# Kernel tuning notes

Hardware: AMD Instinct MI355X
Metric: run time of the kernel (lower is better)

Reference implementation:

```python
import jax, jax.numpy as jnp
import numpy as np

E, V, F, D = 500000, 50000, 100000, 128

def setup_inputs() -> dict:
    key = jax.random.key(0)
    ks = jax.random.split(key, 8)
    return {
        "prev_m_f_to_v": jax.random.normal(ks[0], (E, D), jnp.float32),
        "variable": jax.random.normal(ks[1], (V, D), jnp.float32),
        "factor": jax.random.normal(ks[2], (F, D), jnp.float32),
        "edge_attr": jax.random.normal(ks[3], (E, D), jnp.float32),
        "v_to_f": jax.random.randint(ks[4], (E,), 0, V, jnp.int32),
        "f_to_v": jax.random.randint(ks[5], (E,), 0, F, jnp.int32),
        "Wv": jax.random.normal(ks[6], (3 * D, D), jnp.float32) * (1.0 / np.sqrt(3 * D)),
        "bv": jnp.zeros((D,), jnp.float32),
        "Wf": jax.random.normal(ks[7], (3 * D, D), jnp.float32) * (1.0 / np.sqrt(3 * D)),
        "bf": jnp.zeros((D,), jnp.float32),
    }

def _mlp(x, y, edge_attr, W, b):
    # update(): concat along features then Linear(3d->d) + relu
    h = jnp.concatenate((x, y, edge_attr), axis=-1)  # [E, 3D]
    return jax.nn.relu(h @ W + b)                    # [E, D]

def reference(prev_m_f_to_v, variable, factor, edge_attr, v_to_f, f_to_v, Wv, bv, Wf, bf):
    nV = variable.shape[0]
    nF = factor.shape[0]
    # scatter-sum of factor->variable messages onto variables
    sum_f_to_v = jax.ops.segment_sum(prev_m_f_to_v, v_to_f, num_segments=nV)  # [V, D]
    # BP exclusion: gather back and subtract own message
    m_v_to_f = sum_f_to_v[v_to_f] - prev_m_f_to_v                             # [E, D]
    m_v_to_f = _mlp(variable[v_to_f], m_v_to_f, edge_attr, Wv, bv)            # [E, D]
    # scatter-sum of variable->factor messages onto factors
    sum_v_to_f = jax.ops.segment_sum(m_v_to_f, f_to_v, num_segments=nF)       # [F, D]
    m_f_to_v = sum_v_to_f[f_to_v] - m_v_to_f                                  # [E, D]
    m_f_to_v = _mlp(factor[f_to_v], m_f_to_v, edge_attr, Wf, bf)              # [E, D]
    new_factor = sum_v_to_f + factor
    new_variable = sum_f_to_v + variable
    return (m_f_to_v, new_factor, new_variable)
```

## Files before the change

### kernel.cpp

```cpp
#include <hip/hip_runtime.h>

typedef __attribute__((ext_vector_type(8))) __bf16 bf16x8;
typedef __attribute__((ext_vector_type(4))) __bf16 bf16x4;
typedef __attribute__((ext_vector_type(2))) __bf16 bf16x2;
typedef __attribute__((ext_vector_type(4))) float f32x4;

template <int N> struct ic { static constexpr int value = N; };

__device__ __forceinline__ void gload_lds16(const void* g, void* l) {
    __builtin_amdgcn_global_load_lds(
        (const __attribute__((address_space(1))) void*)g,
        (__attribute__((address_space(3))) void*)l, 16, 0, 0);
}

__device__ inline bf16x8 pack8(f32x4 u0, f32x4 u1) {
    bf16x8 r;
    r[0] = (__bf16)u0[0]; r[1] = (__bf16)u0[1]; r[2] = (__bf16)u0[2]; r[3] = (__bf16)u0[3];
    r[4] = (__bf16)u1[0]; r[5] = (__bf16)u1[1]; r[6] = (__bf16)u1[2]; r[7] = (__bf16)u1[3];
    return r;
}

__global__ void pack_all(const float* __restrict__ Wv, const float* __restrict__ Wf,
                         __bf16* __restrict__ Wtab_v, __bf16* __restrict__ Wedge_v,
                         __bf16* __restrict__ Wtab_f, __bf16* __restrict__ Wedge_f) {
    int which = blockIdx.x >> 7;
    int i = ((blockIdx.x & 127) << 8) + threadIdx.x;
    const float* W = (which < 2) ? Wv : Wf;
    __bf16* out = (which == 0) ? Wtab_v : (which == 1) ? Wedge_v
                 : (which == 2) ? Wtab_f : Wedge_f;
    int baseA = (which & 1) ? 128 : 0;
    float sA  = (which & 1) ? -1.f : 1.f;
    int baseB = (which & 1) ? 256 : 128;
    int k = i >> 7, d = i & 127;
    float v = (k < 128) ? sA * W[(long)(baseA + k) * 128 + d]
                        : W[(long)(baseB + (k - 128)) * 128 + d];
    int t = k >> 5, n = d >> 4;
    int lane = (d & 15) | (((k >> 3) & 3) << 4);
    int j = k & 7;
    out[((long)(t * 8 + n) * 64 + lane) * 8 + j] = (__bf16)v;
}


__global__ void hist_kernel(const int* __restrict__ v_to_f, const int* __restrict__ f_to_v,
                            int* __restrict__ counts, int V, int E) {
    int stride = gridDim.x * blockDim.x;
    for (int e = blockIdx.x * blockDim.x + threadIdx.x; e < E; e += stride) {
        atomicAdd(&counts[v_to_f[e]], 1);
        atomicAdd(&counts[V + f_to_v[e]], 1);
    }
}

#define SCAN_BLOCK 256
#define SCAN_ELEMS 4

__global__ void scan_pass1(const int* __restrict__ counts, int* __restrict__ partials, int N) {
    int t = threadIdx.x;
    int base = blockIdx.x * (SCAN_BLOCK * SCAN_ELEMS) + t * SCAN_ELEMS;
    int s = 0;
#pragma unroll
    for (int j = 0; j < SCAN_ELEMS; ++j) {
        int i = base + j;
        if (i < N) s += counts[i];
    }
#pragma unroll
    for (int off = 1; off < 64; off <<= 1) s += __shfl_xor(s, off);
    __shared__ int lds[4];
    if ((t & 63) == 0) lds[t >> 6] = s;
    __syncthreads();
    if (t == 0) partials[blockIdx.x] = lds[0] + lds[1] + lds[2] + lds[3];
}

__global__ void scan_pass3(const int* __restrict__ counts, const int* __restrict__ partials,
                           int* __restrict__ offsets, int* __restrict__ cursors,
                           int N, int total) {
    int t = threadIdx.x;
    int pre = 0;
    for (int i = 0; i < (int)blockIdx.x; ++i) pre += partials[i];
    int base = blockIdx.x * (SCAN_BLOCK * SCAN_ELEMS) + t * SCAN_ELEMS;
    int c[SCAN_ELEMS];
    int s = 0;
#pragma unroll
    for (int j = 0; j < SCAN_ELEMS; ++j) {
        int i = base + j;
        c[j] = (i < N) ? counts[i] : 0;
        s += c[j];
    }
    int lane = t & 63, w = t >> 6;
    int x = s;
#pragma unroll
    for (int off = 1; off < 64; off <<= 1) { int y = __shfl_up(x, off); if (lane >= off) x += y; }
    __shared__ int lds[4];
    if (lane == 63) lds[w] = x;
    __syncthreads();
    int add = 0;
    for (int i = 0; i < w; ++i) add += lds[i];
    int run = x + add - s + pre;
#pragma unroll
    for (int j = 0; j < SCAN_ELEMS; ++j) {
        int i = base + j;
        if (i < N) { offsets[i] = run; cursors[i] = run; }
        run += c[j];
    }
    if (blockIdx.x == 0 && t == 0) offsets[N] = total;
}

__global__ void fill_kernel(const int* __restrict__ v_to_f, const int* __restrict__ f_to_v,
                            int* __restrict__ cursors, int* __restrict__ bucket, int V, int E) {
    int stride = gridDim.x * blockDim.x;
    for (int e = blockIdx.x * blockDim.x + threadIdx.x; e < E; e += stride) {
        int p = atomicAdd(&cursors[v_to_f[e]], 1);
        bucket[p] = e;
        int q = atomicAdd(&cursors[V + f_to_v[e]], 1);
        bucket[q] = e;
    }
}


__global__ __launch_bounds__(256) void gsum_f32(
    const float* __restrict__ src, const int* __restrict__ bucket,
    const int* __restrict__ offsets, int toff,
    const float* __restrict__ addtab, float* __restrict__ sumout,
    float* __restrict__ addout, int T) {
    int gw = (int)((blockIdx.x * (long)blockDim.x + threadIdx.x) >> 6);
    if (gw >= T) return;
    int lane = threadIdx.x & 63;
    int start = offsets[toff + gw], end = offsets[toff + gw + 1];
    float ax = 0.f, ay = 0.f, bx = 0.f, by = 0.f;
    float cx = 0.f, cy = 0.f, dx = 0.f, dy = 0.f;
    int i = start;
    for (; i + 3 < end; i += 4) {
        int e0 = bucket[i], e1 = bucket[i + 1], e2 = bucket[i + 2], e3 = bucket[i + 3];
        float2 v0 = *(const float2*)(src + (long)e0 * 128 + lane * 2);
        float2 v1 = *(const float2*)(src + (long)e1 * 128 + lane * 2);
        float2 v2 = *(const float2*)(src + (long)e2 * 128 + lane * 2);
        float2 v3 = *(const float2*)(src + (long)e3 * 128 + lane * 2);
        ax += v0.x; ay += v0.y; bx += v1.x; by += v1.y;
        cx += v2.x; cy += v2.y; dx += v3.x; dy += v3.y;
    }
    for (; i < end; ++i) {
        int e0 = bucket[i];
        float2 v0 = *(const float2*)(src + (long)e0 * 128 + lane * 2);
        ax += v0.x; ay += v0.y;
    }
    ax += bx + cx + dx; ay += by + cy + dy;
    long o = (long)gw * 128 + lane * 2;
    *(float2*)(sumout + o) = make_float2(ax, ay);
    float2 a = *(const float2*)(addtab + o);
    *(float2*)(addout + o) = make_float2(ax + a.x, ay + a.y);
}

__global__ __launch_bounds__(256) void gsum_bf16(
    const __bf16* __restrict__ src, const int* __restrict__ bucket,
    const int* __restrict__ offsets, int toff,
    const float* __restrict__ addtab, float* __restrict__ sumout,
    float* __restrict__ addout, int T) {
    int gw = (int)((blockIdx.x * (long)blockDim.x + threadIdx.x) >> 6);
    if (gw >= T) return;
    int lane = threadIdx.x & 63;
    int start = offsets[toff + gw], end = offsets[toff + gw + 1];
    float ax = 0.f, ay = 0.f, bx = 0.f, by = 0.f;
    float cx = 0.f, cy = 0.f, dx = 0.f, dy = 0.f;
    int i = start;
    for (; i + 3 < end; i += 4) {
        int e0 = bucket[i], e1 = bucket[i + 1], e2 = bucket[i + 2], e3 = bucket[i + 3];
        bf16x2 v0 = *(const bf16x2*)(src + (long)e0 * 128 + lane * 2);
        bf16x2 v1 = *(const bf16x2*)(src + (long)e1 * 128 + lane * 2);
        bf16x2 v2 = *(const bf16x2*)(src + (long)e2 * 128 + lane * 2);
        bf16x2 v3 = *(const bf16x2*)(src + (long)e3 * 128 + lane * 2);
        ax += (float)v0[0]; ay += (float)v0[1]; bx += (float)v1[0]; by += (float)v1[1];
        cx += (float)v2[0]; cy += (float)v2[1]; dx += (float)v3[0]; dy += (float)v3[1];
    }
    for (; i < end; ++i) {
        int e0 = bucket[i];
        bf16x2 v0 = *(const bf16x2*)(src + (long)e0 * 128 + lane * 2);
        ax += (float)v0[0]; ay += (float)v0[1];
    }
    ax += bx + cx + dx; ay += by + cy + dy;
    long o = (long)gw * 128 + lane * 2;
    *(float2*)(sumout + o) = make_float2(ax, ay);
    float2 a = *(const float2*)(addtab + o);
    *(float2*)(addout + o) = make_float2(ax + a.x, ay + a.y);
}

__global__ __launch_bounds__(256, 4) void table_gemm(
    const float* __restrict__ src0, const float* __restrict__ src1,
    const __bf16* __restrict__ WT, const float* __restrict__ bias,
    __bf16* __restrict__ out, int T) {
    const int wave = threadIdx.x >> 6;
    const int lane = threadIdx.x & 63;
    const int row = lane & 15;
    const int kch = lane >> 4;
    const long wbase = ((long)blockIdx.x * 4 + wave) * 32;

    const float* p0[2]; const float* p1[2];
#pragma unroll
    for (int rb = 0; rb < 2; ++rb) {
        long r = wbase + rb * 16 + row;
        long rl = (r < T) ? r : (T - 1);
        p0[rb] = src0 + rl * 128 + kch * 8;
        p1[rb] = src1 + rl * 128 + kch * 8;
    }

    f32x4 acc[8][2];
#pragma unroll
    for (int n = 0; n < 8; ++n) {
        acc[n][0] = (f32x4){0.f, 0.f, 0.f, 0.f};
        acc[n][1] = (f32x4){0.f, 0.f, 0.f, 0.f};
    }

#pragma unroll
    for (int t = 0; t < 8; ++t) {
        bf16x8 a[2];
#pragma unroll
        for (int rb = 0; rb < 2; ++rb) {
            const float* p = (t < 4) ? (p0[rb] + t * 32) : (p1[rb] + (t - 4) * 32);
            f32x4 u0 = *(const f32x4*)p;
            f32x4 u1 = *(const f32x4*)(p + 4);
            a[rb] = pack8(u0, u1);
        }
        const __bf16* bbase = WT + (long)t * 8 * 512 + lane * 8;
#pragma unroll
        for (int n = 0; n < 8; ++n) {
            bf16x8 b = *(const bf16x8*)(bbase + n * 512);
            acc[n][0] = __builtin_amdgcn_mfma_f32_16x16x32_bf16(a[0], b, acc[n][0], 0, 0, 0);
            acc[n][1] = __builtin_amdgcn_mfma_f32_16x16x32_bf16(a[1], b, acc[n][1], 0, 0, 0);
        }
    }

    const int colbase = lane & 15;
    const int orow = (lane >> 4) * 4;
#pragma unroll
    for (int n = 0; n < 8; ++n) {
        int col = n * 16 + colbase;
        float bz = bias[col];
#pragma unroll
        for (int rb = 0; rb < 2; ++rb)
#pragma unroll
            for (int rr = 0; rr < 4; ++rr) {
                long r = wbase + rb * 16 + orow + rr;
                if (r < T) out[r * 128 + col] = (__bf16)(acc[n][rb][rr] + bz);
            }
    }
}

template <int PHASE>
__global__ __launch_bounds__(256, 3) void edge_gemm(
    const float* __restrict__ prevf, const __bf16* __restrict__ prevb,
    const float* __restrict__ eattr, const __bf16* __restrict__ WT,
    const __bf16* __restrict__ G, const int* __restrict__ idx,
    __bf16* __restrict__ outb, float* __restrict__ outf, int E) {
    __shared__ char lds[4][12288];
    const int wave = threadIdx.x >> 6;
    const int lane = threadIdx.x & 63;
    const int l16 = lane & 15;
    const int kch = lane >> 4;
    const long brow = (long)blockIdx.x * 128;
    const long wrow = brow + wave * 32;
    char* wls = &lds[wave][0];

    bf16x8 bufA[8], bufB[8];
    f32x4 acc[8][2];
#pragma unroll
    for (int n = 0; n < 8; ++n) {
        acc[n][0] = (f32x4){0.f, 0.f, 0.f, 0.f};
        acc[n][1] = (f32x4){0.f, 0.f, 0.f, 0.f};
    }

    auto stage = [&](auto tcS) {
        constexpr int S = decltype(tcS)::value;
        char* dst = wls + (S % 3) * 4096;
        if constexpr (PHASE == 2 && S < 4) {
#pragma unroll
            for (int q = 0; q < 2; ++q) {
                int row = q * 16 + (lane >> 2);
                int c2 = (lane & 3) ^ ((row >> 1) & 3);
                long rg = wrow + row; if (rg >= E) rg = E - 1;
                gload_lds16(prevb + rg * 128 + S * 32 + c2 * 8, dst + q * 1024);
            }
        } else {
            const float* srcb = (PHASE == 1 && S < 4) ? (prevf + S * 32)
                                                      : (eattr + (S - 4) * 32);
#pragma unroll
            for (int q = 0; q < 4; ++q) {
                int row = q * 8 + (lane >> 3);
                int c2 = (lane & 7) ^ (row & 7);
                long rg = wrow + row; if (rg >= E) rg = E - 1;
                gload_lds16(srcb + rg * 128 + c2 * 4, dst + q * 1024);
            }
        }
    };

    auto loadB = [&](auto tcT, bf16x8* bn) {
        constexpr int T = decltype(tcT)::value;
        const __bf16* bb = WT + (long)T * 4096 + lane * 8;
#pragma unroll
        for (int n = 0; n < 8; ++n) bn[n] = *(const bf16x8*)(bb + n * 512);
    };

    stage(ic<0>{});
    __builtin_amdgcn_sched_barrier(0);
    loadB(ic<0>{}, bufA);
    __builtin_amdgcn_sched_barrier(0);
    stage(ic<1>{});
    __builtin_amdgcn_sched_barrier(0);

    auto iter = [&](auto tcT) {
        constexpr int T = decltype(tcT)::value;
        constexpr int NS = (T < 7) ? (8 + ((PHASE == 2 && (T + 1) < 4) ? 2 : 4)) : 8;
        asm volatile("s_waitcnt vmcnt(%0)" :: "n"(NS) : "memory");
        __builtin_amdgcn_sched_barrier(0);
        if constexpr (T < 7) loadB(ic<T + 1>{}, (T & 1) ? bufA : bufB);
        __builtin_amdgcn_sched_barrier(0);
        if constexpr (T < 6) stage(ic<T + 2>{});
        __builtin_amdgcn_sched_barrier(0);
        const char* cur = wls + (T % 3) * 4096;
        bf16x8 a[2];
#pragma unroll
        for (int rb = 0; rb < 2; ++rb) {
            int row = rb * 16 + l16;
            if constexpr (PHASE == 2 && T < 4) {
                a[rb] = *(const bf16x8*)(cur + row * 64 + ((kch ^ ((row >> 1) & 3)) * 16));
            } else {
                f32x4 u0 = *(const f32x4*)(cur + row * 128 + (((kch * 2) ^ (row & 7)) * 16));
                f32x4 u1 = *(const f32x4*)(cur + row * 128 + (((kch * 2 + 1) ^ (row & 7)) * 16));
                a[rb] = pack8(u0, u1);
            }
        }
        bf16x8* bc = (T & 1) ? bufB : bufA;
#pragma unroll
        for (int n = 0; n < 8; ++n) {
            acc[n][0] = __builtin_amdgcn_mfma_f32_16x16x32_bf16(a[0], bc[n], acc[n][0], 0, 0, 0);
            acc[n][1] = __builtin_amdgcn_mfma_f32_16x16x32_bf16(a[1], bc[n], acc[n][1], 0, 0, 0);
        }
    };
    iter(ic<0>{}); iter(ic<1>{}); iter(ic<2>{}); iter(ic<3>{});
    iter(ic<4>{}); iter(ic<5>{}); iter(ic<6>{}); iter(ic<7>{});

    float* lbuf = (float*)wls;
    const int slotcol = lane & 31;
    const int rhalf = lane >> 5;
#pragma unroll
    for (int rb = 0; rb < 2; ++rb) {
#pragma unroll
        for (int n = 0; n < 8; ++n)
#pragma unroll
            for (int rr = 0; rr < 4; ++rr) {
                int row = kch * 4 + rr;
                int col = n * 16 + l16;
                int slot = col >> 2;
                lbuf[row * 128 + (((slot ^ (row & 7)) << 2) | (col & 3))] = acc[n][rb][rr];
            }
#pragma unroll
        for (int j = 0; j < 8; ++j) {
            int row = 2 * j + rhalf;
            long eo = wrow + rb * 16 + row;
            f32x4 v = *(const f32x4*)&lbuf[row * 128 + ((slotcol ^ (row & 7)) << 2)];
            if (eo < E) {
                int g = idx[eo];
                bf16x4 gb = *(const bf16x4*)(G + (long)g * 128 + slotcol * 4);
                f32x4 o;
#pragma unroll
                for (int i = 0; i < 4; ++i) {
                    float x = v[i] + (float)gb[i];
                    o[i] = x > 0.f ? x : 0.f;
                }
                if (PHASE == 1) {
                    bf16x4 ob;
#pragma unroll
                    for (int i = 0; i < 4; ++i) ob[i] = (__bf16)o[i];
                    *(bf16x4*)(outb + eo * 128 + slotcol * 4) = ob;
                } else {
                    *(f32x4*)(outf + eo * 128 + slotcol * 4) = o;
                }
            }
        }
    }
}

extern "C" void kernel_launch(void* const* d_in, const int* in_sizes, int n_in,
                              void* d_out, int out_size, void* d_ws, size_t ws_size,
                              hipStream_t stream) {
    const float* prev_m   = (const float*)d_in[0];
    const float* variable = (const float*)d_in[1];
    const float* factor   = (const float*)d_in[2];
    const float* eattr    = (const float*)d_in[3];
    const int*   v_to_f   = (const int*)d_in[4];
    const int*   f_to_v   = (const int*)d_in[5];
    const float* Wv       = (const float*)d_in[6];
    const float* bv       = (const float*)d_in[7];
    const float* Wf       = (const float*)d_in[8];
    const float* bf       = (const float*)d_in[9];

    const int E = in_sizes[0] / 128;
    const int V = in_sizes[1] / 128;
    const int F = in_sizes[2] / 128;
    const int NT = V + F;

    float* out_m        = (float*)d_out;
    float* out_factor   = out_m + (long)E * 128;
    float* out_variable = out_factor + (long)F * 128;

    char* ws = (char*)d_ws;
    float* sum_f_to_v = (float*)ws;  ws += (long)V * 128 * 4;
    float* sum_v_to_f = (float*)ws;  ws += (long)F * 128 * 4;
    __bf16* m1        = (__bf16*)ws; ws += (long)E * 128 * 2;
    __bf16* G1        = (__bf16*)ws; ws += (long)V * 128 * 2;
    __bf16* G2        = (__bf16*)ws; ws += (long)F * 128 * 2;
    __bf16* Wtab_v    = (__bf16*)ws; ws += 256 * 128 * 2;
    __bf16* Wedge_v   = (__bf16*)ws; ws += 256 * 128 * 2;
    __bf16* Wtab_f    = (__bf16*)ws; ws += 256 * 128 * 2;
    __bf16* Wedge_f   = (__bf16*)ws; ws += 256 * 128 * 2;
    int* counts       = (int*)ws;    ws += (long)NT * 4;
    int* offsets      = (int*)ws;    ws += (long)(NT + 1) * 4;
    int* cursors      = (int*)ws;    ws += (long)NT * 4;
    int* bucket       = (int*)ws;    ws += (long)2 * E * 4;
    int* partials     = (int*)ws;    ws += 256 * 4;

    hipMemsetAsync(counts, 0, (size_t)NT * 4, stream);

    pack_all<<<dim3(512), dim3(256), 0, stream>>>(Wv, Wf, Wtab_v, Wedge_v, Wtab_f, Wedge_f);

    hist_kernel<<<dim3(2048), dim3(256), 0, stream>>>(v_to_f, f_to_v, counts, V, E);
    int nb = (NT + SCAN_BLOCK * SCAN_ELEMS - 1) / (SCAN_BLOCK * SCAN_ELEMS);
    scan_pass1<<<dim3(nb), dim3(SCAN_BLOCK), 0, stream>>>(counts, partials, NT);
    scan_pass3<<<dim3(nb), dim3(SCAN_BLOCK), 0, stream>>>(counts, partials, offsets, cursors,
                                                          NT, 2 * E);
    fill_kernel<<<dim3(2048), dim3(256), 0, stream>>>(v_to_f, f_to_v, cursors, bucket, V, E);

    gsum_f32<<<dim3((V + 3) / 4), dim3(256), 0, stream>>>(
        prev_m, bucket, offsets, 0, variable, sum_f_to_v, out_variable, V);

    table_gemm<<<dim3((V + 127) / 128), dim3(256), 0, stream>>>(
        variable, sum_f_to_v, Wtab_v, bv, G1, V);

    int eblocks = (E + 127) / 128;
    edge_gemm<1><<<dim3(eblocks), dim3(256), 0, stream>>>(
        prev_m, nullptr, eattr, Wedge_v, G1, v_to_f, m1, nullptr, E);

    gsum_bf16<<<dim3((F + 3) / 4), dim3(256), 0, stream>>>(
        m1, bucket, offsets, V, factor, sum_v_to_f, out_factor, F);

    table_gemm<<<dim3((F + 127) / 128), dim3(256), 0, stream>>>(
        factor, sum_v_to_f, Wtab_f, bf, G2, F);

    edge_gemm<2><<<dim3(eblocks), dim3(256), 0, stream>>>(
        nullptr, m1, eattr, Wedge_f, G2, f_to_v, nullptr, out_m, E);
}
```

Measured before the change: 713.4 us.

## Restructure edge GEMM pipeline with inline-asm LDS reads and move table adds

Inside edge_gemm, the A-tile LDS reads are now issued as explicit ds_read_b128 instructions with a single lgkmcnt wait. The B-fragment register loads are moved to after the MFMAs and prefetch two iterations ahead instead of one. Separately, the residual adds (sum + variable/factor) move out of the gather-sum kernels and into the tail of table_gemm, which already reads both sources. The intent is better overlap of global loads with MFMA work and lighter gather kernels. The risks are extra register pressure and a reordered waitcnt schedule in the hot kernel.

```diff
diff --git a/kernel.cpp b/kernel.cpp
--- a/kernel.cpp
+++ b/kernel.cpp
@@ -11,6 +11,22 @@
     __builtin_amdgcn_global_load_lds(
         (const __attribute__((address_space(1))) void*)g,
         (__attribute__((address_space(3))) void*)l, 16, 0, 0);
+}
+
+__device__ __forceinline__ unsigned lds_addr(const void* p) {
+    return (unsigned)(unsigned long long)(__attribute__((address_space(3))) const char*)p;
+}
+
+__device__ __forceinline__ f32x4 ds_read_b128_f(unsigned a) {
+    f32x4 r;
+    asm volatile("ds_read_b128 %0, %1" : "=v"(r) : "v"(a));
+    return r;
+}
+
+__device__ __forceinline__ bf16x8 ds_read_b128_h(unsigned a) {
+    bf16x8 r;
+    asm volatile("ds_read_b128 %0, %1" : "=v"(r) : "v"(a));
+    return r;
 }
 
 __device__ inline bf16x8 pack8(f32x4 u0, f32x4 u1) {
@@ -119,8 +135,7 @@
 __global__ __launch_bounds__(256) void gsum_f32(
     const float* __restrict__ src, const int* __restrict__ bucket,
     const int* __restrict__ offsets, int toff,
-    const float* __restrict__ addtab, float* __restrict__ sumout,
-    float* __restrict__ addout, int T) {
+    float* __restrict__ sumout, int T) {
     int gw = (int)((blockIdx.x * (long)blockDim.x + threadIdx.x) >> 6);
     if (gw >= T) return;
     int lane = threadIdx.x & 63;
@@ -145,15 +160,12 @@
     ax += bx + cx + dx; ay += by + cy + dy;
     long o = (long)gw * 128 + lane * 2;
     *(float2*)(sumout + o) = make_float2(ax, ay);
-    float2 a = *(const float2*)(addtab + o);
-    *(float2*)(addout + o) = make_float2(ax + a.x, ay + a.y);
 }
 
 __global__ __launch_bounds__(256) void gsum_bf16(
     const __bf16* __restrict__ src, const int* __restrict__ bucket,
     const int* __restrict__ offsets, int toff,
-    const float* __restrict__ addtab, float* __restrict__ sumout,
-    float* __restrict__ addout, int T) {
+    float* __restrict__ sumout, int T) {
     int gw = (int)((blockIdx.x * (long)blockDim.x + threadIdx.x) >> 6);
     if (gw >= T) return;
     int lane = threadIdx.x & 63;
@@ -178,14 +190,12 @@
     ax += bx + cx + dx; ay += by + cy + dy;
     long o = (long)gw * 128 + lane * 2;
     *(float2*)(sumout + o) = make_float2(ax, ay);
-    float2 a = *(const float2*)(addtab + o);
-    *(float2*)(addout + o) = make_float2(ax + a.x, ay + a.y);
 }
 
 __global__ __launch_bounds__(256, 4) void table_gemm(
     const float* __restrict__ src0, const float* __restrict__ src1,
     const __bf16* __restrict__ WT, const float* __restrict__ bias,
-    __bf16* __restrict__ out, int T) {
+    __bf16* __restrict__ out, float* __restrict__ addout, int T) {
     const int wave = threadIdx.x >> 6;
     const int lane = threadIdx.x & 63;
     const int row = lane & 15;
@@ -240,6 +250,22 @@
                 long r = wbase + rb * 16 + orow + rr;
                 if (r < T) out[r * 128 + col] = (__bf16)(acc[n][rb][rr] + bz);
             }
+    }
+
+    const long eb = (long)blockIdx.x * 128 * 128;
+#pragma unroll
+    for (int j = 0; j < 16; ++j) {
+        int vec = j * 256 + threadIdx.x;
+        long r = (long)blockIdx.x * 128 + (vec >> 5);
+        if (r < T) {
+            long off = eb + (long)vec * 4;
+            f32x4 x = *(const f32x4*)(src0 + off);
+            f32x4 y = *(const f32x4*)(src1 + off);
+            f32x4 o;
+            o[0] = x[0] + y[0]; o[1] = x[1] + y[1];
+            o[2] = x[2] + y[2]; o[3] = x[3] + y[3];
+            *(f32x4*)(addout + off) = o;
+        }
     }
 }
 
@@ -257,6 +283,7 @@
     const long brow = (long)blockIdx.x * 128;
     const long wrow = brow + wave * 32;
     char* wls = &lds[wave][0];
+    const unsigned wlsa = lds_addr(wls);
 
     bf16x8 bufA[8], bufB[8];
     f32x4 acc[8][2];
@@ -303,38 +330,49 @@
     __builtin_amdgcn_sched_barrier(0);
     stage(ic<1>{});
     __builtin_amdgcn_sched_barrier(0);
+    loadB(ic<1>{}, bufB);
+    __builtin_amdgcn_sched_barrier(0);
 
     auto iter = [&](auto tcT) {
         constexpr int T = decltype(tcT)::value;
-        constexpr int NS = (T < 7) ? (8 + ((PHASE == 2 && (T + 1) < 4) ? 2 : 4)) : 8;
+        constexpr int LS1 = (PHASE == 2 && (T + 1) < 4) ? 2 : 4;
+        constexpr int NS = (T < 7) ? (8 + LS1) : 0;
         asm volatile("s_waitcnt vmcnt(%0)" :: "n"(NS) : "memory");
         __builtin_amdgcn_sched_barrier(0);
-        if constexpr (T < 7) loadB(ic<T + 1>{}, (T & 1) ? bufA : bufB);
+        const unsigned cb = wlsa + (T % 3) * 4096;
+        bf16x8 a[2];
+        if constexpr (PHASE == 2 && T < 4) {
+            const int r0 = l16, r1 = 16 + l16;
+            bf16x8 h0 = ds_read_b128_h(cb + r0 * 64 + ((kch ^ ((r0 >> 1) & 3)) * 16));
+            bf16x8 h1 = ds_read_b128_h(cb + r1 * 64 + ((kch ^ ((r1 >> 1) & 3)) * 16));
+            asm volatile("s_waitcnt lgkmcnt(0)" ::: "memory");
+            __builtin_amdgcn_sched_barrier(0);
+            a[0] = h0; a[1] = h1;
+        } else {
+            const int r0 = l16, r1 = 16 + l16;
+            f32x4 u0 = ds_read_b128_f(cb + r0 * 128 + (((kch * 2) ^ (r0 & 7)) * 16));
+            f32x4 u1 = ds_read_b128_f(cb + r0 * 128 + (((kch * 2 + 1) ^ (r0 & 7)) * 16));
+            f32x4 u2 = ds_read_b128_f(cb + r1 * 128 + (((kch * 2) ^ (r1 & 7)) * 16));
+            f32x4 u3 = ds_read_b128_f(cb + r1 * 128 + (((kch * 2 + 1) ^ (r1 & 7)) * 16));
+            asm volatile("s_waitcnt lgkmcnt(0)" ::: "memory");
+            __builtin_amdgcn_sched_barrier(0);
+            a[0] = pack8(u0, u1); a[1] = pack8(u2, u3);
+        }
+        if constexpr (T + 2 < 8) stage(ic<T + 2>{});
         __builtin_amdgcn_sched_barrier(0);
-        if constexpr (T < 6) stage(ic<T + 2>{});
-        __builtin_amdgcn_sched_barrier(0);
-        const char* cur = wls + (T % 3) * 4096;
-        bf16x8 a[2];
-#pragma unroll
-        for (int rb = 0; rb < 2; ++rb) {
-            int row = rb * 16 + l16;
-            if constexpr (PHASE == 2 && T < 4) {
-                a[rb] = *(const bf16x8*)(cur + row * 64 + ((kch ^ ((row >> 1) & 3)) * 16));
-            } else {
-                f32x4 u0 = *(const f32x4*)(cur + row * 128 + (((kch * 2) ^ (row & 7)) * 16));
-                f32x4 u1 = *(const f32x4*)(cur + row * 128 + (((kch * 2 + 1) ^ (row & 7)) * 16));
-                a[rb] = pack8(u0, u1);
-            }
-        }
         bf16x8* bc = (T & 1) ? bufB : bufA;
 #pragma unroll
         for (int n = 0; n < 8; ++n) {
             acc[n][0] = __builtin_amdgcn_mfma_f32_16x16x32_bf16(a[0], bc[n], acc[n][0], 0, 0, 0);
             acc[n][1] = __builtin_amdgcn_mfma_f32_16x16x32_bf16(a[1], bc[n], acc[n][1], 0, 0, 0);
         }
+        __builtin_amdgcn_sched_barrier(0);
+        if constexpr (T + 2 < 8) loadB(ic<T + 2>{}, (T & 1) ? bufB : bufA);
+        __builtin_amdgcn_sched_barrier(0);
     };
     iter(ic<0>{}); iter(ic<1>{}); iter(ic<2>{}); iter(ic<3>{});
     iter(ic<4>{}); iter(ic<5>{}); iter(ic<6>{}); iter(ic<7>{});
+    __builtin_amdgcn_sched_barrier(0);
 
     float* lbuf = (float*)wls;
     const int slotcol = lane & 31;
@@ -428,20 +466,20 @@
     fill_kernel<<<dim3(2048), dim3(256), 0, stream>>>(v_to_f, f_to_v, cursors, bucket, V, E);
 
     gsum_f32<<<dim3((V + 3) / 4), dim3(256), 0, stream>>>(
-        prev_m, bucket, offsets, 0, variable, sum_f_to_v, out_variable, V);
+        prev_m, bucket, offsets, 0, sum_f_to_v, V);
 
     table_gemm<<<dim3((V + 127) / 128), dim3(256), 0, stream>>>(
-        variable, sum_f_to_v, Wtab_v, bv, G1, V);
+        variable, sum_f_to_v, Wtab_v, bv, G1, out_variable, V);
 
     int eblocks = (E + 127) / 128;
     edge_gemm<1><<<dim3(eblocks), dim3(256), 0, stream>>>(
         prev_m, nullptr, eattr, Wedge_v, G1, v_to_f, m1, nullptr, E);
 
     gsum_bf16<<<dim3((F + 3) / 4), dim3(256), 0, stream>>>(
-        m1, bucket, offsets, V, factor, sum_v_to_f, out_factor, F);
+        m1, bucket, offsets, V, sum_v_to_f, F);
 
     table_gemm<<<dim3((F + 127) / 128), dim3(256), 0, stream>>>(
-        factor, sum_v_to_f, Wtab_f, bf, G2, F);
+        factor, sum_v_to_f, Wtab_f, bf, G2, out_factor, F);
 
     edge_gemm<2><<<dim3(eblocks), dim3(256), 0, stream>>>(
         nullptr, m1, eattr, Wedge_f, G2, f_to_v, nullptr, out_m, E);
```

Result: slower. 788.4 us (+10.5%).
